# Performance work log

Measured on AMD Instinct MI355X. Metric: run time of the kernel, lower is better.

The kernel has to match this reference:

```python
import jax, jax.numpy as jnp
import numpy as np
from jax import lax

V, D, H = 32000, 512, 512  # vocab, embedding_dim, hidden_size (must match for the DxD matmul chain)
B, T, A = 64, 256, 4       # batch, sentence len, aspect len
EPS = 1e-5


def setup_inputs() -> dict:
    key = jax.random.key(0)
    ks = jax.random.split(key, 12)
    sc = 0.05
    return {
        "x": jax.random.randint(ks[0], (B, T), 0, V),
        "s": jax.random.randint(ks[1], (B, A), 0, V),
        "embed": jax.random.normal(ks[2], (V, D), jnp.float32) * sc,
        "W_ih": jax.random.normal(ks[3], (4 * H, D), jnp.float32) * sc,
        "W_hh": jax.random.normal(ks[4], (4 * H, H), jnp.float32) * sc,
        "b_lstm": jax.random.normal(ks[5], (4 * H,), jnp.float32) * sc,
        "w_y": jax.random.normal(ks[6], (D, D), jnp.float32) * sc,
        "w_t": jax.random.normal(ks[7], (D, D), jnp.float32) * sc,
        "w_p": jax.random.normal(ks[8], (D, D), jnp.float32) * sc,
        "w_x": jax.random.normal(ks[9], (D, D), jnp.float32) * sc,
        "w_f": jax.random.normal(ks[10], (D, D), jnp.float32) * sc,
        "b_f": jax.random.normal(ks[11], (D,), jnp.float32) * sc,
    }


def _lstm(emb, W_ih, W_hh, b):
    # emb: [B, T, D] -> hidden states [B, T, H]; PyTorch gate order i,f,g,o
    Bx = emb.shape[0]
    Hh = W_hh.shape[1]
    h0 = jnp.zeros((Bx, Hh), emb.dtype)
    c0 = jnp.zeros((Bx, Hh), emb.dtype)

    def step(carry, x_t):
        h, c = carry
        z = x_t @ W_ih.T + h @ W_hh.T + b  # [B, 4H]
        i, f, g, o = jnp.split(z, 4, axis=-1)
        c = jax.nn.sigmoid(f) * c + jax.nn.sigmoid(i) * jnp.tanh(g)
        h = jax.nn.sigmoid(o) * jnp.tanh(c)
        return (h, c), h

    _, hs = lax.scan(step, (h0, c0), jnp.swapaxes(emb, 0, 1))
    return jnp.swapaxes(hs, 0, 1)  # [B, T, H]


def reference(x, s, embed, W_ih, W_hh, b_lstm, w_y, w_t, w_p, w_x, w_f, b_f):
    # 1) embed + LSTM over the sentence
    emb = embed[x]                      # [B, T, D]
    Hs = _lstm(emb, W_ih, W_hh, b_lstm)  # [B, T, H]

    # 2) aspect: embed, batch-normalize per feature, sum over aspect tokens
    s_emb = embed[s]                    # [B, A, D]
    mu = s_emb.mean(axis=(0, 1))
    var = s_emb.var(axis=(0, 1))
    s_norm = ((s_emb - mu) * lax.rsqrt(var + EPS)).sum(axis=1)  # [B, D]

    # 3) FFT circular correlation: m_t = ifft(fft(h_t) * conj(fft(s))).real
    Hf = jnp.fft.fft(Hs, axis=-1)                      # [B, T, D] complex
    Sf = jnp.conj(jnp.fft.fft(s_norm, axis=-1))        # [B, D]
    m = jnp.fft.ifft(Hf * Sf[:, None, :], axis=-1).real.astype(Hs.dtype)  # [B, T, D]

    # 4) attention chain
    Y = jnp.tanh(jnp.einsum('de,bte->btd', w_y, m))            # [B, T, D]
    alpha = jax.nn.softmax(jnp.einsum('de,bte->btd', w_t, Y), axis=1)  # softmax over time
    r = jnp.einsum('btd,btd->bd', alpha, Hs)                   # [B, D]
    h_star = jnp.tanh(r @ w_p.T + Hs[:, -1] @ w_x.T)           # [B, D]
    return jax.nn.softmax(h_star @ w_f.T + b_f, axis=-1)       # [B, D]
```

## Files before the change

### kernel.cpp

```cpp
#include <hip/hip_runtime.h>


typedef __bf16 bf16x8 __attribute__((ext_vector_type(8)));
typedef float f32x4 __attribute__((ext_vector_type(4)));

#define B_ 64
#define T_ 256
#define D_ 512
#define H4 2048

__device__ __forceinline__ unsigned short f2bf(float f) {
    unsigned u = __float_as_uint(f);
    u += 0x7fffu + ((u >> 16) & 1u);
    return (unsigned short)(u >> 16);
}
__device__ __forceinline__ float bf2f(unsigned short x) {
    return __uint_as_float(((unsigned)x) << 16);
}
__device__ __forceinline__ float bf2f_lo(unsigned u) { return __uint_as_float(u << 16); }
__device__ __forceinline__ float bf2f_hi(unsigned u) { return __uint_as_float(u & 0xffff0000u); }

__device__ __forceinline__ float frcp(float x) { return __builtin_amdgcn_rcpf(x); }
__device__ __forceinline__ float fast_sigmoid(float x) {
    return frcp(1.f + __expf(-x));
}
__device__ __forceinline__ float fast_tanh(float x) {
    return 1.f - 2.f * frcp(1.f + __expf(2.f * x));
}

__global__ __launch_bounds__(256)
void gemm_bt(const void* __restrict__ Abase, int a_f32,
             const int* __restrict__ gather_idx,
             const float* __restrict__ Bmat,
             const float* __restrict__ circ_src,
             const float* __restrict__ bias,
             unsigned short* __restrict__ outb,
             float* __restrict__ outf,
             int N, int K,
             long A_bstride, long out_bstride,
             int act)
{
    __shared__ __align__(16) unsigned short Asm[128 * 40];
    __shared__ __align__(16) unsigned short Bsm[128 * 40];

    const int bz = blockIdx.z;
    const int tile_n = blockIdx.x * 128;
    const int tile_m = blockIdx.y * 128;
    const int tid = threadIdx.x;
    const int lane = tid & 63;
    const int w = tid >> 6;
    const int wm = (w >> 1) * 64;
    const int wn = (w & 1) * 64;

    const int srow = tid >> 1;
    const int skc = (tid & 1) * 16;

    const float* arow_f = nullptr;
    const unsigned short* arow_h = nullptr;
    if (a_f32) {
        const float* Af = (const float*)Abase;
        if (gather_idx) arow_f = Af + (long)gather_idx[tile_m + srow] * K;
        else            arow_f = Af + (long)bz * A_bstride + (long)(tile_m + srow) * K;
    } else {
        arow_h = (const unsigned short*)Abase + (long)bz * A_bstride + (long)(tile_m + srow) * K;
    }
    const float* brow = nullptr;
    const float* csrc = nullptr;
    if (circ_src) csrc = circ_src + bz * 512;
    else brow = Bmat + (long)(tile_n + srow) * K;

    f32x4 zero4 = {0.f, 0.f, 0.f, 0.f};
    f32x4 acc[4][4];
    #pragma unroll
    for (int mi = 0; mi < 4; mi++)
        #pragma unroll
        for (int ni = 0; ni < 4; ni++) acc[mi][ni] = zero4;

    const int fr = lane & 15;
    const int fq = (lane >> 4) * 8;

    for (int kc = 0; kc < K; kc += 32) {
        __syncthreads();
        if (a_f32) {
            float4 u0 = *(const float4*)(arow_f + kc + skc);
            float4 u1 = *(const float4*)(arow_f + kc + skc + 4);
            float4 u2 = *(const float4*)(arow_f + kc + skc + 8);
            float4 u3 = *(const float4*)(arow_f + kc + skc + 12);
            unsigned short tmp[16] __attribute__((aligned(16)));
            tmp[0] = f2bf(u0.x); tmp[1] = f2bf(u0.y); tmp[2]  = f2bf(u0.z); tmp[3]  = f2bf(u0.w);
            tmp[4] = f2bf(u1.x); tmp[5] = f2bf(u1.y); tmp[6]  = f2bf(u1.z); tmp[7]  = f2bf(u1.w);
            tmp[8] = f2bf(u2.x); tmp[9] = f2bf(u2.y); tmp[10] = f2bf(u2.z); tmp[11] = f2bf(u2.w);
            tmp[12] = f2bf(u3.x); tmp[13] = f2bf(u3.y); tmp[14] = f2bf(u3.z); tmp[15] = f2bf(u3.w);
            *(uint4*)&Asm[srow * 40 + skc]     = *(const uint4*)tmp;
            *(uint4*)&Asm[srow * 40 + skc + 8] = *(const uint4*)(tmp + 8);
        } else {
            *(uint4*)&Asm[srow * 40 + skc]     = *(const uint4*)(arow_h + kc + skc);
            *(uint4*)&Asm[srow * 40 + skc + 8] = *(const uint4*)(arow_h + kc + skc + 8);
        }
        if (csrc) {
            unsigned short tmp[16] __attribute__((aligned(16)));
            int n_abs = tile_n + srow;
            #pragma unroll
            for (int j = 0; j < 16; j++) {
                int k_abs = kc + skc + j;
                tmp[j] = f2bf(csrc[(k_abs - n_abs) & 511]);
            }
            *(uint4*)&Bsm[srow * 40 + skc]     = *(const uint4*)tmp;
            *(uint4*)&Bsm[srow * 40 + skc + 8] = *(const uint4*)(tmp + 8);
        } else {
            float4 u0 = *(const float4*)(brow + kc + skc);
            float4 u1 = *(const float4*)(brow + kc + skc + 4);
            float4 u2 = *(const float4*)(brow + kc + skc + 8);
            float4 u3 = *(const float4*)(brow + kc + skc + 12);
            unsigned short tmp[16] __attribute__((aligned(16)));
            tmp[0] = f2bf(u0.x); tmp[1] = f2bf(u0.y); tmp[2]  = f2bf(u0.z); tmp[3]  = f2bf(u0.w);
            tmp[4] = f2bf(u1.x); tmp[5] = f2bf(u1.y); tmp[6]  = f2bf(u1.z); tmp[7]  = f2bf(u1.w);
            tmp[8] = f2bf(u2.x); tmp[9] = f2bf(u2.y); tmp[10] = f2bf(u2.z); tmp[11] = f2bf(u2.w);
            tmp[12] = f2bf(u3.x); tmp[13] = f2bf(u3.y); tmp[14] = f2bf(u3.z); tmp[15] = f2bf(u3.w);
            *(uint4*)&Bsm[srow * 40 + skc]     = *(const uint4*)tmp;
            *(uint4*)&Bsm[srow * 40 + skc + 8] = *(const uint4*)(tmp + 8);
        }
        __syncthreads();
        bf16x8 av[4], bv[4];
        #pragma unroll
        for (int mi = 0; mi < 4; mi++)
            av[mi] = *(const bf16x8*)&Asm[(wm + mi * 16 + fr) * 40 + fq];
        #pragma unroll
        for (int ni = 0; ni < 4; ni++)
            bv[ni] = *(const bf16x8*)&Bsm[(wn + ni * 16 + fr) * 40 + fq];
        #pragma unroll
        for (int mi = 0; mi < 4; mi++)
            #pragma unroll
            for (int ni = 0; ni < 4; ni++)
                acc[mi][ni] = __builtin_amdgcn_mfma_f32_16x16x32_bf16(
                    av[mi], bv[ni], acc[mi][ni], 0, 0, 0);
    }

    #pragma unroll
    for (int mi = 0; mi < 4; mi++) {
        #pragma unroll
        for (int ni = 0; ni < 4; ni++) {
            #pragma unroll
            for (int rg = 0; rg < 4; rg++) {
                int row = tile_m + wm + mi * 16 + (lane >> 4) * 4 + rg;
                int col = tile_n + wn + ni * 16 + (lane & 15);
                float v = acc[mi][ni][rg];
                if (bias) v += bias[col];
                if (act == 1) v = fast_tanh(v);
                long oidx = (long)bz * out_bstride + (long)row * N + col;
                if (outb) outb[oidx] = f2bf(v);
                else outf[oidx] = v;
            }
        }
    }
}

#define WSTRIDE 520
#define SENT 0xFFFFFFFFu
#define ZL(g,r,d) zl[((g)*16+(r))*33+(d)]

__global__ __launch_bounds__(512)
void persistent_lstm(const float* __restrict__ Whh,
                     const unsigned short* __restrict__ Zx,
                     unsigned int* __restrict__ Hsu)
{
    __shared__ __align__(16) unsigned short hsm[16 * WSTRIDE];
    __shared__ float zl[4 * 16 * 33];

    const int bg = blockIdx.x >> 4;
    const int nb = blockIdx.x & 15;
    const int tid = threadIdx.x;
    const int w = tid >> 6;
    const int lane = tid & 63;
    const int fr = lane & 15;
    const int fq = (lane >> 4) * 8;
    const int g = w >> 1;
    const int f = w & 1;

    bf16x8 wfrag[16];
    {
        const float* wrow = Whh + (long)(g * 512 + nb * 32 + f * 16 + fr) * 512;
        #pragma unroll
        for (int c = 0; c < 16; c++) {
            int k0 = c * 32 + fq;
            float4 u0 = *(const float4*)(wrow + k0);
            float4 u1 = *(const float4*)(wrow + k0 + 4);
            unsigned short tmp[8] __attribute__((aligned(16)));
            tmp[0] = f2bf(u0.x); tmp[1] = f2bf(u0.y); tmp[2] = f2bf(u0.z); tmp[3] = f2bf(u0.w);
            tmp[4] = f2bf(u1.x); tmp[5] = f2bf(u1.y); tmp[6] = f2bf(u1.z); tmp[7] = f2bf(u1.w);
            wfrag[c] = *(const bf16x8*)tmp;
        }
    }

    int st_r[8], st_dp[8];
    #pragma unroll
    for (int it = 0; it < 8; it++) {
        int idx = it * 512 + tid;
        st_r[it] = idx >> 8;
        st_dp[it] = idx & 255;
    }

    const int grow = (tid & 255) >> 4;
    const int d0 = (tid & 15) * 2;
    const int b_own = bg * 16 + grow;
    const int dg = nb * 32 + d0;
    float ca = 0.f, cb = 0.f;

    f32x4 zero4 = {0.f, 0.f, 0.f, 0.f};

    for (int t = 0; t < T_; t++) {
        unsigned zi_u = 0, zf_u = 0, zg_u = 0, zo_u = 0;
        if (tid < 256) {
            const long zb = ((long)b_own * T_ + t) * H4 + dg;
            zi_u = *(const unsigned*)&Zx[zb + 0 * 512];
            zf_u = *(const unsigned*)&Zx[zb + 1 * 512];
            zg_u = *(const unsigned*)&Zx[zb + 2 * 512];
            zo_u = *(const unsigned*)&Zx[zb + 3 * 512];
        }

        f32x4 acc = zero4;
        if (t > 0) {
            unsigned vv[8];
            long ad[8];
            #pragma unroll
            for (int it = 0; it < 8; it++) {
                ad[it] = ((long)(bg * 16 + st_r[it]) * T_ + (t - 1)) * 256 + st_dp[it];
                vv[it] = __hip_atomic_load(Hsu + ad[it], __ATOMIC_RELAXED,
                                           __HIP_MEMORY_SCOPE_AGENT);
            }
            while (true) {
                bool pend = false;
                #pragma unroll
                for (int it = 0; it < 8; it++) pend |= (vv[it] == SENT);
                if (!__ballot(pend)) break;
                #pragma unroll
                for (int it = 0; it < 8; it++) {
                    vv[it] = __hip_atomic_load(Hsu + ad[it], __ATOMIC_RELAXED,
                                               __HIP_MEMORY_SCOPE_AGENT);
                }
            }
            #pragma unroll
            for (int it = 0; it < 8; it++) {
                *(unsigned*)&hsm[st_r[it] * WSTRIDE + st_dp[it] * 2] = vv[it];
            }
            __syncthreads();
            const unsigned short* arow = hsm + fr * WSTRIDE;
            f32x4 ac0 = zero4, ac1 = zero4, ac2 = zero4, ac3 = zero4;
            #pragma unroll
            for (int c = 0; c < 16; c += 4) {
                bf16x8 x0 = *(const bf16x8*)(arow + (c + 0) * 32 + fq);
                bf16x8 x1 = *(const bf16x8*)(arow + (c + 1) * 32 + fq);
                bf16x8 x2 = *(const bf16x8*)(arow + (c + 2) * 32 + fq);
                bf16x8 x3 = *(const bf16x8*)(arow + (c + 3) * 32 + fq);
                ac0 = __builtin_amdgcn_mfma_f32_16x16x32_bf16(x0, wfrag[c + 0], ac0, 0, 0, 0);
                ac1 = __builtin_amdgcn_mfma_f32_16x16x32_bf16(x1, wfrag[c + 1], ac1, 0, 0, 0);
                ac2 = __builtin_amdgcn_mfma_f32_16x16x32_bf16(x2, wfrag[c + 2], ac2, 0, 0, 0);
                ac3 = __builtin_amdgcn_mfma_f32_16x16x32_bf16(x3, wfrag[c + 3], ac3, 0, 0, 0);
            }
            acc = (ac0 + ac1) + (ac2 + ac3);
        }
        {
            const int q4 = (lane >> 4) * 4;
            const int cl = f * 16 + (lane & 15);
            #pragma unroll
            for (int rg = 0; rg < 4; rg++) {
                ZL(g, q4 + rg, cl) = acc[rg];
            }
        }
        __syncthreads();
        if (tid < 256) {
            float zi0 = ZL(0, grow, d0)     + bf2f_lo(zi_u);
            float zi1 = ZL(0, grow, d0 + 1) + bf2f_hi(zi_u);
            float zf0 = ZL(1, grow, d0)     + bf2f_lo(zf_u);
            float zf1 = ZL(1, grow, d0 + 1) + bf2f_hi(zf_u);
            float zg0 = ZL(2, grow, d0)     + bf2f_lo(zg_u);
            float zg1 = ZL(2, grow, d0 + 1) + bf2f_hi(zg_u);
            float zo0 = ZL(3, grow, d0)     + bf2f_lo(zo_u);
            float zo1 = ZL(3, grow, d0 + 1) + bf2f_hi(zo_u);

            ca = fast_sigmoid(zf0) * ca + fast_sigmoid(zi0) * fast_tanh(zg0);
            cb = fast_sigmoid(zf1) * cb + fast_sigmoid(zi1) * fast_tanh(zg1);
            float h0 = fast_sigmoid(zo0) * fast_tanh(ca);
            float h1 = fast_sigmoid(zo1) * fast_tanh(cb);

            unsigned hp = (unsigned)f2bf(h0) | ((unsigned)f2bf(h1) << 16);
            __hip_atomic_store(Hsu + ((long)b_own * T_ + t) * 256 + nb * 16 + (tid & 15),
                               hp, __ATOMIC_RELAXED, __HIP_MEMORY_SCOPE_AGENT);
        }
    }
}

__global__ __launch_bounds__(64)
void aspect_norm(const int* __restrict__ s,
                 const float* __restrict__ embed,
                 float* __restrict__ s_norm)
{
    __shared__ int sidx[256];
    const int tid = threadIdx.x;
    const int d = blockIdx.x * 64 + tid;
    for (int i = tid; i < 256; i += 64) sidx[i] = s[i];
    __syncthreads();
    float sum = 0.f, sq = 0.f;
    for (int i = 0; i < 256; i++) {
        float v = embed[(long)sidx[i] * D_ + d];
        sum += v; sq += v * v;
    }
    float mu = sum * (1.f / 256.f);
    float var = sq * (1.f / 256.f) - mu * mu;
    float rstd = rsqrtf(var + 1e-5f);
    for (int b = 0; b < 64; b++) {
        float acc = 0.f;
        #pragma unroll
        for (int a = 0; a < 4; a++) {
            acc += embed[(long)sidx[b * 4 + a] * D_ + d] - mu;
        }
        s_norm[b * D_ + d] = acc * rstd;
    }
}

__global__ __launch_bounds__(256)
void attn_r(const float* __restrict__ apre,
            const unsigned short* __restrict__ Hs,
            float* __restrict__ r)
{
    const int b = blockIdx.y;
    const int d = blockIdx.x * 256 + threadIdx.x;
    const float* ap = apre + (long)b * T_ * D_ + d;
    const unsigned short* hp = Hs + (long)b * T_ * D_ + d;
    float mx = ap[0], sm = 1.f;
    for (int t = 1; t < T_; t++) {
        float v = ap[(long)t * D_];
        if (v > mx) { sm = sm * __expf(mx - v) + 1.f; mx = v; }
        else sm += __expf(v - mx);
    }
    float acc = 0.f;
    for (int t = 0; t < T_; t++) {
        acc += __expf(ap[(long)t * D_] - mx) * bf2f(hp[(long)t * D_]);
    }
    r[b * D_ + d] = acc / sm;
}

__global__ __launch_bounds__(256)
void hstar_kernel(const float* __restrict__ r,
                  const unsigned short* __restrict__ Hs,
                  const float* __restrict__ w_p,
                  const float* __restrict__ w_x,
                  float* __restrict__ h_star)
{
    __shared__ float rs[512];
    __shared__ float hts[512];
    const int b = blockIdx.x, tid = threadIdx.x;
    const long hlast = ((long)b * T_ + (T_ - 1)) * D_;
    rs[tid] = r[b * D_ + tid];
    rs[tid + 256] = r[b * D_ + 256 + tid];
    hts[tid] = bf2f(Hs[hlast + tid]);
    hts[tid + 256] = bf2f(Hs[hlast + 256 + tid]);
    __syncthreads();
    for (int d = tid; d < 512; d += 256) {
        const float* wp = w_p + (long)d * D_;
        const float* wx = w_x + (long)d * D_;
        float acc = 0.f;
        for (int e = 0; e < 512; e += 4) {
            float4 p1 = *(const float4*)(wp + e);
            float4 p2 = *(const float4*)(wx + e);
            acc += p1.x * rs[e] + p1.y * rs[e + 1] + p1.z * rs[e + 2] + p1.w * rs[e + 3];
            acc += p2.x * hts[e] + p2.y * hts[e + 1] + p2.z * hts[e + 2] + p2.w * hts[e + 3];
        }
        h_star[b * D_ + d] = fast_tanh(acc);
    }
}

__global__ __launch_bounds__(256)
void out_kernel(const float* __restrict__ h_star,
                const float* __restrict__ w_f,
                const float* __restrict__ b_f,
                float* __restrict__ out)
{
    __shared__ float hs[512];
    __shared__ float lg[512];
    __shared__ float red[8];
    const int b = blockIdx.x, tid = threadIdx.x;
    hs[tid] = h_star[b * D_ + tid];
    hs[tid + 256] = h_star[b * D_ + 256 + tid];
    __syncthreads();
    for (int d = tid; d < 512; d += 256) {
        const float* wr = w_f + (long)d * D_;
        float acc = b_f[d];
        for (int e = 0; e < 512; e += 4) {
            float4 p = *(const float4*)(wr + e);
            acc += p.x * hs[e] + p.y * hs[e + 1] + p.z * hs[e + 2] + p.w * hs[e + 3];
        }
        lg[d] = acc;
    }
    __syncthreads();
    float m0 = fmaxf(lg[tid], lg[tid + 256]);
    for (int off = 32; off > 0; off >>= 1) m0 = fmaxf(m0, __shfl_down(m0, off, 64));
    if ((tid & 63) == 0) red[tid >> 6] = m0;
    __syncthreads();
    float bmax = fmaxf(fmaxf(red[0], red[1]), fmaxf(red[2], red[3]));
    float e0 = __expf(lg[tid] - bmax);
    float e1 = __expf(lg[tid + 256] - bmax);
    float s0 = e0 + e1;
    for (int off = 32; off > 0; off >>= 1) s0 += __shfl_down(s0, off, 64);
    if ((tid & 63) == 0) red[4 + (tid >> 6)] = s0;
    __syncthreads();
    float inv = 1.f / (red[4] + red[5] + red[6] + red[7]);
    out[b * D_ + tid] = e0 * inv;
    out[b * D_ + 256 + tid] = e1 * inv;
}

extern "C" void kernel_launch(void* const* d_in, const int* in_sizes, int n_in,
                              void* d_out, int out_size, void* d_ws, size_t ws_size,
                              hipStream_t stream)
{
    (void)in_sizes; (void)n_in; (void)out_size; (void)ws_size;

    const int* x = (const int*)d_in[0];
    const int* s = (const int*)d_in[1];
    const float* embed  = (const float*)d_in[2];
    const float* W_ih   = (const float*)d_in[3];
    const float* W_hh   = (const float*)d_in[4];
    const float* b_lstm = (const float*)d_in[5];
    const float* w_y = (const float*)d_in[6];
    const float* w_t = (const float*)d_in[7];
    const float* w_p = (const float*)d_in[8];
    const float* w_x = (const float*)d_in[9];
    const float* w_f = (const float*)d_in[10];
    const float* b_f = (const float*)d_in[11];

    char* ws = (char*)d_ws;
    unsigned short* Zx   = (unsigned short*)(ws + 0);
    float*          apre = (float*)(ws + 0);
    unsigned short* mbuf = (unsigned short*)(ws + 33554432);
    unsigned short* Ybuf = (unsigned short*)(ws + 50331648);
    unsigned short* Hs   = (unsigned short*)(ws + 67108864);
    float* s_norm = (float*)(ws + 86114304);
    float* rbuf   = (float*)(ws + 86245376);
    float* hstar  = (float*)(ws + 86376448);

    hipMemsetAsync(Hs, 0xFF, (size_t)B_ * T_ * D_ * 2, stream);

    aspect_norm<<<dim3(8), dim3(64), 0, stream>>>(s, embed, s_norm);

    gemm_bt<<<dim3(16, 128, 1), dim3(256), 0, stream>>>(
        embed, 1, x, W_ih, nullptr, b_lstm, Zx, nullptr,
        2048, 512, 0L, 0L, 0);

    persistent_lstm<<<dim3(64), dim3(512), 0, stream>>>(
        W_hh, Zx, (unsigned int*)Hs);


    gemm_bt<<<dim3(4, 2, 64), dim3(256), 0, stream>>>(
        Hs, 0, nullptr, nullptr, s_norm, nullptr, mbuf, nullptr,
        512, 512, (long)(T_ * D_), (long)(T_ * D_), 0);

    gemm_bt<<<dim3(4, 128, 1), dim3(256), 0, stream>>>(
        mbuf, 0, nullptr, w_y, nullptr, nullptr, Ybuf, nullptr,
        512, 512, 0L, 0L, 1);

    gemm_bt<<<dim3(4, 128, 1), dim3(256), 0, stream>>>(
        Ybuf, 0, nullptr, w_t, nullptr, nullptr, nullptr, apre,
        512, 512, 0L, 0L, 0);

    attn_r<<<dim3(2, 64), dim3(256), 0, stream>>>(apre, Hs, rbuf);

    hstar_kernel<<<dim3(64), dim3(256), 0, stream>>>(rbuf, Hs, w_p, w_x, hstar);

    out_kernel<<<dim3(64), dim3(256), 0, stream>>>(hstar, w_f, b_f, (float*)d_out);
}
```

Measured before the change: 1.095 ms.

## Repartition persistent LSTM blocks to 8 batch rows by 64 hidden units

```diff
diff --git a/kernel.cpp b/kernel.cpp
--- a/kernel.cpp
+++ b/kernel.cpp
@@ -157,18 +157,18 @@
 
 #define WSTRIDE 520
 #define SENT 0xFFFFFFFFu
-#define ZL(g,r,d) zl[((g)*16+(r))*33+(d)]
-
-__global__ __launch_bounds__(512)
+#define ZL(g,r,d) zl[((g)*8+(r))*65+(d)]
+
+__global__ __launch_bounds__(512, 2)
 void persistent_lstm(const float* __restrict__ Whh,
                      const unsigned short* __restrict__ Zx,
                      unsigned int* __restrict__ Hsu)
 {
     __shared__ __align__(16) unsigned short hsm[16 * WSTRIDE];
-    __shared__ float zl[4 * 16 * 33];
-
-    const int bg = blockIdx.x >> 4;
-    const int nb = blockIdx.x & 15;
+    __shared__ float zl[4 * 8 * 65];
+
+    const int cq  = blockIdx.x & 7;
+    const int nbp = blockIdx.x >> 3;
     const int tid = threadIdx.x;
     const int w = tid >> 6;
     const int lane = tid & 63;
@@ -177,9 +177,10 @@
     const int g = w >> 1;
     const int f = w & 1;
 
-    bf16x8 wfrag[16];
-    {
-        const float* wrow = Whh + (long)(g * 512 + nb * 32 + f * 16 + fr) * 512;
+    bf16x8 wfrag[2][16];
+    #pragma unroll
+    for (int n = 0; n < 2; n++) {
+        const float* wrow = Whh + (long)(g * 512 + nbp * 64 + f * 32 + n * 16 + fr) * 512;
         #pragma unroll
         for (int c = 0; c < 16; c++) {
             int k0 = c * 32 + fq;
@@ -188,22 +189,25 @@
             unsigned short tmp[8] __attribute__((aligned(16)));
             tmp[0] = f2bf(u0.x); tmp[1] = f2bf(u0.y); tmp[2] = f2bf(u0.z); tmp[3] = f2bf(u0.w);
             tmp[4] = f2bf(u1.x); tmp[5] = f2bf(u1.y); tmp[6] = f2bf(u1.z); tmp[7] = f2bf(u1.w);
-            wfrag[c] = *(const bf16x8*)tmp;
-        }
-    }
-
-    int st_r[8], st_dp[8];
+            wfrag[n][c] = *(const bf16x8*)tmp;
+        }
+    }
+
+    for (int i = tid; i < 16 * WSTRIDE / 2; i += 512)
+        ((unsigned*)hsm)[i] = 0;
+
+    int st_r[4], st_dp[4];
     #pragma unroll
-    for (int it = 0; it < 8; it++) {
-        int idx = it * 512 + tid;
-        st_r[it] = idx >> 8;
-        st_dp[it] = idx & 255;
-    }
-
-    const int grow = (tid & 255) >> 4;
-    const int d0 = (tid & 15) * 2;
-    const int b_own = bg * 16 + grow;
-    const int dg = nb * 32 + d0;
+    for (int k = 0; k < 4; k++) {
+        int idx = k * 512 + tid;
+        st_r[k] = idx >> 8;
+        st_dp[k] = idx & 255;
+    }
+
+    const int grow = (tid & 255) >> 5;
+    const int d0 = (tid & 31) * 2;
+    const int b_own = cq * 8 + grow;
+    const int dg = nbp * 64 + d0;
     float ca = 0.f, cb = 0.f;
 
     f32x4 zero4 = {0.f, 0.f, 0.f, 0.f};
@@ -218,53 +222,60 @@
             zo_u = *(const unsigned*)&Zx[zb + 3 * 512];
         }
 
-        f32x4 acc = zero4;
+        f32x4 an0 = zero4, an1 = zero4;
         if (t > 0) {
-            unsigned vv[8];
-            long ad[8];
-            #pragma unroll
-            for (int it = 0; it < 8; it++) {
-                ad[it] = ((long)(bg * 16 + st_r[it]) * T_ + (t - 1)) * 256 + st_dp[it];
-                vv[it] = __hip_atomic_load(Hsu + ad[it], __ATOMIC_RELAXED,
-                                           __HIP_MEMORY_SCOPE_AGENT);
+            unsigned vv[4];
+            long ad[4];
+            #pragma unroll
+            for (int k = 0; k < 4; k++) {
+                ad[k] = ((long)(cq * 8 + st_r[k]) * T_ + (t - 1)) * 256 + st_dp[k];
+                vv[k] = __hip_atomic_load(Hsu + ad[k], __ATOMIC_RELAXED,
+                                          __HIP_MEMORY_SCOPE_AGENT);
             }
             while (true) {
                 bool pend = false;
                 #pragma unroll
-                for (int it = 0; it < 8; it++) pend |= (vv[it] == SENT);
+                for (int k = 0; k < 4; k++) pend |= (vv[k] == SENT);
                 if (!__ballot(pend)) break;
                 #pragma unroll
-                for (int it = 0; it < 8; it++) {
-                    vv[it] = __hip_atomic_load(Hsu + ad[it], __ATOMIC_RELAXED,
-                                               __HIP_MEMORY_SCOPE_AGENT);
+                for (int k = 0; k < 4; k++) {
+                    vv[k] = __hip_atomic_load(Hsu + ad[k], __ATOMIC_RELAXED,
+                                              __HIP_MEMORY_SCOPE_AGENT);
                 }
             }
             #pragma unroll
-            for (int it = 0; it < 8; it++) {
-                *(unsigned*)&hsm[st_r[it] * WSTRIDE + st_dp[it] * 2] = vv[it];
+            for (int k = 0; k < 4; k++) {
+                *(unsigned*)&hsm[st_r[k] * WSTRIDE + st_dp[k] * 2] = vv[k];
             }
             __syncthreads();
             const unsigned short* arow = hsm + fr * WSTRIDE;
-            f32x4 ac0 = zero4, ac1 = zero4, ac2 = zero4, ac3 = zero4;
+            f32x4 a0[4] = {zero4, zero4, zero4, zero4};
+            f32x4 a1[4] = {zero4, zero4, zero4, zero4};
             #pragma unroll
             for (int c = 0; c < 16; c += 4) {
                 bf16x8 x0 = *(const bf16x8*)(arow + (c + 0) * 32 + fq);
                 bf16x8 x1 = *(const bf16x8*)(arow + (c + 1) * 32 + fq);
                 bf16x8 x2 = *(const bf16x8*)(arow + (c + 2) * 32 + fq);
                 bf16x8 x3 = *(const bf16x8*)(arow + (c + 3) * 32 + fq);
-                ac0 = __builtin_amdgcn_mfma_f32_16x16x32_bf16(x0, wfrag[c + 0], ac0, 0, 0, 0);
-                ac1 = __builtin_amdgcn_mfma_f32_16x16x32_bf16(x1, wfrag[c + 1], ac1, 0, 0, 0);
-                ac2 = __builtin_amdgcn_mfma_f32_16x16x32_bf16(x2, wfrag[c + 2], ac2, 0, 0, 0);
-                ac3 = __builtin_amdgcn_mfma_f32_16x16x32_bf16(x3, wfrag[c + 3], ac3, 0, 0, 0);
-            }
-            acc = (ac0 + ac1) + (ac2 + ac3);
-        }
-        {
-            const int q4 = (lane >> 4) * 4;
-            const int cl = f * 16 + (lane & 15);
+                a0[0] = __builtin_amdgcn_mfma_f32_16x16x32_bf16(x0, wfrag[0][c + 0], a0[0], 0, 0, 0);
+                a0[1] = __builtin_amdgcn_mfma_f32_16x16x32_bf16(x1, wfrag[0][c + 1], a0[1], 0, 0, 0);
+                a0[2] = __builtin_amdgcn_mfma_f32_16x16x32_bf16(x2, wfrag[0][c + 2], a0[2], 0, 0, 0);
+                a0[3] = __builtin_amdgcn_mfma_f32_16x16x32_bf16(x3, wfrag[0][c + 3], a0[3], 0, 0, 0);
+                a1[0] = __builtin_amdgcn_mfma_f32_16x16x32_bf16(x0, wfrag[1][c + 0], a1[0], 0, 0, 0);
+                a1[1] = __builtin_amdgcn_mfma_f32_16x16x32_bf16(x1, wfrag[1][c + 1], a1[1], 0, 0, 0);
+                a1[2] = __builtin_amdgcn_mfma_f32_16x16x32_bf16(x2, wfrag[1][c + 2], a1[2], 0, 0, 0);
+                a1[3] = __builtin_amdgcn_mfma_f32_16x16x32_bf16(x3, wfrag[1][c + 3], a1[3], 0, 0, 0);
+            }
+            an0 = (a0[0] + a0[1]) + (a0[2] + a0[3]);
+            an1 = (a1[0] + a1[1]) + (a1[2] + a1[3]);
+        }
+        if (lane < 32) {
+            const int rb = (lane >> 4) * 4;
+            const int cl = f * 32 + (lane & 15);
             #pragma unroll
             for (int rg = 0; rg < 4; rg++) {
-                ZL(g, q4 + rg, cl) = acc[rg];
+                ZL(g, rb + rg, cl)      = an0[rg];
+                ZL(g, rb + rg, cl + 16) = an1[rg];
             }
         }
         __syncthreads();
@@ -284,7 +295,7 @@
             float h1 = fast_sigmoid(zo1) * fast_tanh(cb);
 
             unsigned hp = (unsigned)f2bf(h0) | ((unsigned)f2bf(h1) << 16);
-            __hip_atomic_store(Hsu + ((long)b_own * T_ + t) * 256 + nb * 16 + (tid & 15),
+            __hip_atomic_store(Hsu + ((long)b_own * T_ + t) * 256 + nbp * 32 + (tid & 31),
                                hp, __ATOMIC_RELAXED, __HIP_MEMORY_SCOPE_AGENT);
         }
     }
```

Result: faster. 1.043 ms (-4.7%).
